# Performance work log

Hardware: AMD Instinct MI355X
Metric: run time of the kernel (lower is better)

The kernel has to match this reference:

```python
import jax, jax.numpy as jnp
import numpy as np
from jax import lax

NMS_SIZE = 5
THR = 0.0
B, C, H, W = 8, 1, 2048, 2048
# fixed capacity for the jit-compatible nonzero (padded with -1); generous upper
# bound on number of surviving local maxima (~HW/25 per map, half above thr=0)
MAX_KEYPOINTS = 2_000_000


def setup_inputs() -> dict:
    key = jax.random.key(0)
    scores = jax.random.normal(key, (B, C, H, W), dtype=jnp.float32)
    return {"scores": scores}


def _local_max(scores):
    # MaxPool2d(kernel=5, stride=1, padding=2) == SAME-padded windowed max
    return lax.reduce_window(
        scores,
        -jnp.inf,
        lax.max,
        window_dimensions=(1, 1, NMS_SIZE, NMS_SIZE),
        window_strides=(1, 1, 1, 1),
        padding="SAME",
    )


def reference(scores):
    maxima = (scores == _local_max(scores)) & (scores > THR)  # [B,C,H,W] bool
    # torch: maxima.nonzero().t()[2:4] -> (row, col) coordinates of survivors.
    # jit-compatible fixed-size nonzero, padded with -1 (extra entries beyond
    # the true count are fill values, matching a compacted index list).
    _, _, hh, ww = jnp.nonzero(maxima, size=MAX_KEYPOINTS, fill_value=-1)
    return jnp.stack([hh, ww])  # [2, MAX_KEYPOINTS] int
```

## Files before the change

kernel.cpp:

```cpp
#include <hip/hip_runtime.h>
#include <stdint.h>
#include <math.h>

#define BATCH 8
#define HH 2048
#define WW 2048
#define NTOT (BATCH * HH * WW)
#define NWORDS (NTOT / 32)
#define R 16
#define NSTRIPS (HH / R)
#define NBLK (NSTRIPS * BATCH)
#define BLK_WORDS (R * WW / 32)
#define MAXK 2000000
#define TAILBLK ((MAXK / 4 + 255) / 256)

__global__ __launch_bounds__(256) void nms_mask(const float* __restrict__ scores,
                                                uint8_t* __restrict__ maskbytes,
                                                int* __restrict__ counts) {
    const int strip = blockIdx.x;
    const int b     = blockIdx.y;
    const int tid   = threadIdx.x;
    const int lane  = tid & 63;
    const int wv    = tid >> 6;
    const int c0    = wv * 512 + lane * 8;
    const int h0    = strip * R;
    const float* img  = scores + (size_t)b * HH * WW;
    const float* colp = img + c0;

    const bool has_l = (c0 != 0);
    const bool has_r = (c0 != WW - 8);

    float win[5][12];

#define LOAD_ROW(PH, hrow)                                                    \
    do {                                                                      \
        const int h_ = (hrow);                                                \
        if ((unsigned)h_ < (unsigned)HH) {                                    \
            const float* p_ = colp + (size_t)h_ * WW;                         \
            float4 a_ = *(const float4*)(p_);                                 \
            float4 b_ = *(const float4*)(p_ + 4);                             \
            win[PH][2] = a_.x; win[PH][3] = a_.y;                             \
            win[PH][4] = a_.z; win[PH][5] = a_.w;                             \
            win[PH][6] = b_.x; win[PH][7] = b_.y;                             \
            win[PH][8] = b_.z; win[PH][9] = b_.w;                             \
            if (has_l) {                                                      \
                float2 hl_ = *(const float2*)(p_ - 2);                        \
                win[PH][0] = hl_.x; win[PH][1] = hl_.y;                       \
            } else { win[PH][0] = -INFINITY; win[PH][1] = -INFINITY; }        \
            if (has_r) {                                                      \
                float2 hr_ = *(const float2*)(p_ + 8);                        \
                win[PH][10] = hr_.x; win[PH][11] = hr_.y;                     \
            } else { win[PH][10] = -INFINITY; win[PH][11] = -INFINITY; }      \
        } else {                                                              \
            _Pragma("unroll")                                                 \
            for (int k_ = 0; k_ < 12; ++k_) win[PH][k_] = -INFINITY;          \
        }                                                                     \
    } while (0)

    LOAD_ROW(0, h0 - 2);
    LOAD_ROW(1, h0 - 1);
    LOAD_ROW(2, h0 + 0);
    LOAD_ROW(3, h0 + 1);

    int pc = 0;
    size_t outbyte = (((size_t)(b * HH + h0) * WW) + c0) >> 3;

#pragma unroll
    for (int i = 0; i < R; ++i) {
        LOAD_ROW((4 + i) % 5, h0 + 2 + i);
        const int CEN = (2 + i) % 5;

        float v[12];
#pragma unroll
        for (int k = 0; k < 12; ++k)
            v[k] = fmaxf(fmaxf(fmaxf(win[0][k], win[1][k]),
                               fmaxf(win[2][k], win[3][k])), win[4][k]);
        float p[11];
#pragma unroll
        for (int k = 0; k < 11; ++k) p[k] = fmaxf(v[k], v[k + 1]);

        uint32_t byte = 0;
#pragma unroll
        for (int j = 0; j < 8; ++j) {
            const float hm = fmaxf(fmaxf(p[j], p[j + 2]), v[j + 4]);
            const float s  = win[CEN][j + 2];
            if ((s == hm) && (s > 0.0f)) byte |= (1u << j);
        }
        maskbytes[outbyte] = (uint8_t)byte;
        outbyte += WW / 8;
        pc += __popc(byte);
    }
#undef LOAD_ROW

#pragma unroll
    for (int d = 32; d >= 1; d >>= 1) pc += __shfl_down(pc, d, 64);
    __shared__ int wsum[4];
    if (lane == 0) wsum[wv] = pc;
    __syncthreads();
    if (tid == 0) counts[b * NSTRIPS + strip] = wsum[0] + wsum[1] + wsum[2] + wsum[3];
}

__device__ __forceinline__ int block_sum(int v, int tid) {
    const int lane = tid & 63, wv = tid >> 6;
#pragma unroll
    for (int d = 32; d >= 1; d >>= 1) v += __shfl_down(v, d, 64);
    __shared__ int ws[4];
    __shared__ int res;
    if (lane == 0) ws[wv] = v;
    __syncthreads();
    if (tid == 0) res = ws[0] + ws[1] + ws[2] + ws[3];
    __syncthreads();
    return res;
}

__global__ __launch_bounds__(256) void compact_tail(const uint32_t* __restrict__ bitmask,
                                                    const int* __restrict__ counts,
                                                    int* __restrict__ out_h,
                                                    int* __restrict__ out_w) {
    const int tid = threadIdx.x;

    if (blockIdx.x >= NBLK) {
        const uint4 c4 = ((const uint4*)counts)[tid];
        int total = block_sum((int)(c4.x + c4.y + c4.z + c4.w), tid);
        if (total < 0) total = 0;
        if (total > MAXK) total = MAXK;

        const int base = ((int)(blockIdx.x - NBLK) * 256 + tid) * 4;
        if (base >= MAXK) return;
        if (base + 4 <= total) return;

        if (base >= total) {
            const int4 neg = make_int4(-1, -1, -1, -1);
            *(int4*)(out_h + base) = neg;
            *(int4*)(out_w + base) = neg;
        } else {
#pragma unroll
            for (int j = 0; j < 4; ++j) {
                const int idx = base + j;
                if (idx >= total) { out_h[idx] = -1; out_w[idx] = -1; }
            }
        }
        return;
    }

    const int chunk = blockIdx.x;

    const uint4 c4 = ((const uint4*)counts)[tid];
    const int i0 = tid * 4;
    int contrib = 0;
    contrib += (i0 + 0 < chunk) ? (int)c4.x : 0;
    contrib += (i0 + 1 < chunk) ? (int)c4.y : 0;
    contrib += (i0 + 2 < chunk) ? (int)c4.z : 0;
    contrib += (i0 + 3 < chunk) ? (int)c4.w : 0;
    const int chunk_base = block_sum(contrib, tid);

    const uint32_t* base = bitmask + (size_t)chunk * BLK_WORDS;
    uint4 m = ((const uint4*)base)[tid];
    uint32_t words[4] = {m.x, m.y, m.z, m.w};
    int pc = __popc(m.x) + __popc(m.y) + __popc(m.z) + __popc(m.w);

    const int lane = tid & 63, wv = tid >> 6;
    int incl = pc;
#pragma unroll
    for (int d = 1; d < 64; d <<= 1) {
        int n = __shfl_up(incl, d, 64);
        if (lane >= d) incl += n;
    }
    __shared__ int wsums[4];
    if (lane == 63) wsums[wv] = incl;
    __syncthreads();
    int wbase = 0;
    for (int i = 0; i < wv; ++i) wbase += wsums[i];

    int off = chunk_base + wbase + (incl - pc);

    uint32_t idx0 = ((uint32_t)chunk * BLK_WORDS + (uint32_t)tid * 4u) * 32u;
#pragma unroll
    for (int wj = 0; wj < 4; ++wj) {
        uint32_t mm = words[wj];
        const uint32_t ib = idx0 + (uint32_t)wj * 32u;
        while (mm) {
            const int bit = __ffs(mm) - 1;
            mm &= mm - 1;
            const uint32_t idx = ib + bit;
            if (off < MAXK) {
                out_h[off] = (int)((idx >> 11) & 2047);
                out_w[off] = (int)(idx & 2047);
            }
            ++off;
        }
    }
}

extern "C" void kernel_launch(void* const* d_in, const int* in_sizes, int n_in,
                              void* d_out, int out_size, void* d_ws, size_t ws_size,
                              hipStream_t stream) {
    const float* scores = (const float*)d_in[0];
    int* out = (int*)d_out;

    uint32_t* bitmask = (uint32_t*)d_ws;
    int* counts = (int*)((char*)d_ws + (size_t)NWORDS * 4);

    nms_mask<<<dim3(NSTRIPS, BATCH), 256, 0, stream>>>(scores, (uint8_t*)bitmask, counts);
    compact_tail<<<NBLK + TAILBLK, 256, 0, stream>>>(bitmask, counts, out, out + MAXK);
}
```

Baseline: 42.90 us.

## Fuse mask and compaction into one kernel with decoupled look-back scan

Merges the NMS mask kernel and the compaction/tail kernel into a single kernel. The bitmask stays in LDS instead of a global workspace, and chunk offsets come from a decoupled look-back prefix scan over atomic flags, with a dynamic chunk id taken from an atomic counter. The -1 tail fill is spread across all blocks after they spin-wait on the last chunk's inclusive total. This removes one launch and the global bitmask round-trip, but adds a memset, spin-waits and serialization along the look-back chain.

```diff
diff --git a/kernel.cpp b/kernel.cpp
--- a/kernel.cpp
+++ b/kernel.cpp
@@ -5,28 +5,41 @@
 #define BATCH 8
 #define HH 2048
 #define WW 2048
-#define NTOT (BATCH * HH * WW)
-#define NWORDS (NTOT / 32)
 #define R 16
 #define NSTRIPS (HH / R)
 #define NBLK (NSTRIPS * BATCH)
-#define BLK_WORDS (R * WW / 32)
+#define CHUNK_DWORDS (R * WW / 32)
 #define MAXK 2000000
-#define TAILBLK ((MAXK / 4 + 255) / 256)
-
-__global__ __launch_bounds__(256) void nms_mask(const float* __restrict__ scores,
-                                                uint8_t* __restrict__ maskbytes,
-                                                int* __restrict__ counts) {
-    const int strip = blockIdx.x;
-    const int b     = blockIdx.y;
-    const int tid   = threadIdx.x;
-    const int lane  = tid & 63;
-    const int wv    = tid >> 6;
+#define TAIL_I4 (MAXK / 4)
+#define TAIL_PER_BLK ((TAIL_I4 + NBLK - 1) / NBLK)
+
+#define STAT_AGG (1u << 30)
+#define STAT_INC (2u << 30)
+#define VALMASK  0x3FFFFFFFu
+
+__global__ __launch_bounds__(256) void nms_fused(const float* __restrict__ scores,
+                                                 uint32_t* __restrict__ flags,
+                                                 int* __restrict__ out_h,
+                                                 int* __restrict__ out_w) {
+    __shared__ uint32_t lds_mask[CHUNK_DWORDS];
+    __shared__ int wsum[4];
+    __shared__ int bcast[2];
+    __shared__ int vbid_s;
+
+    const int tid  = threadIdx.x;
+    const int lane = tid & 63;
+    const int wv   = tid >> 6;
+
+    if (tid == 0) vbid_s = (int)atomicAdd(&flags[NBLK], 1u);
+    __syncthreads();
+    const int chunk = vbid_s;
+
+    const int b     = chunk >> 7;
+    const int strip = chunk & (NSTRIPS - 1);
+    const int h0    = strip * R;
     const int c0    = wv * 512 + lane * 8;
-    const int h0    = strip * R;
     const float* img  = scores + (size_t)b * HH * WW;
     const float* colp = img + c0;
-
     const bool has_l = (c0 != 0);
     const bool has_r = (c0 != WW - 8);
 
@@ -62,8 +75,8 @@
     LOAD_ROW(2, h0 + 0);
     LOAD_ROW(3, h0 + 1);
 
-    int pc = 0;
-    size_t outbyte = (((size_t)(b * HH + h0) * WW) + c0) >> 3;
+    uint8_t* mbytes = (uint8_t*)lds_mask;
+    const int bytecol = wv * 64 + lane;
 
 #pragma unroll
     for (int i = 0; i < R; ++i) {
@@ -86,49 +99,111 @@
             const float s  = win[CEN][j + 2];
             if ((s == hm) && (s > 0.0f)) byte |= (1u << j);
         }
-        maskbytes[outbyte] = (uint8_t)byte;
-        outbyte += WW / 8;
-        pc += __popc(byte);
+        mbytes[i * 256 + bytecol] = (uint8_t)byte;
     }
 #undef LOAD_ROW
 
-#pragma unroll
-    for (int d = 32; d >= 1; d >>= 1) pc += __shfl_down(pc, d, 64);
-    __shared__ int wsum[4];
-    if (lane == 0) wsum[wv] = pc;
-    __syncthreads();
-    if (tid == 0) counts[b * NSTRIPS + strip] = wsum[0] + wsum[1] + wsum[2] + wsum[3];
-}
-
-__device__ __forceinline__ int block_sum(int v, int tid) {
-    const int lane = tid & 63, wv = tid >> 6;
-#pragma unroll
-    for (int d = 32; d >= 1; d >>= 1) v += __shfl_down(v, d, 64);
-    __shared__ int ws[4];
-    __shared__ int res;
-    if (lane == 0) ws[wv] = v;
-    __syncthreads();
-    if (tid == 0) res = ws[0] + ws[1] + ws[2] + ws[3];
-    __syncthreads();
-    return res;
-}
-
-__global__ __launch_bounds__(256) void compact_tail(const uint32_t* __restrict__ bitmask,
-                                                    const int* __restrict__ counts,
-                                                    int* __restrict__ out_h,
-                                                    int* __restrict__ out_w) {
-    const int tid = threadIdx.x;
-
-    if (blockIdx.x >= NBLK) {
-        const uint4 c4 = ((const uint4*)counts)[tid];
-        int total = block_sum((int)(c4.x + c4.y + c4.z + c4.w), tid);
-        if (total < 0) total = 0;
-        if (total > MAXK) total = MAXK;
-
-        const int base = ((int)(blockIdx.x - NBLK) * 256 + tid) * 4;
-        if (base >= MAXK) return;
-        if (base + 4 <= total) return;
-
+    __syncthreads();
+
+    const uint4 m = ((const uint4*)lds_mask)[tid];
+    const int pc = __popc(m.x) + __popc(m.y) + __popc(m.z) + __popc(m.w);
+
+    int red = pc;
+#pragma unroll
+    for (int d = 32; d >= 1; d >>= 1) red += __shfl_down(red, d, 64);
+    if (lane == 0) wsum[wv] = red;
+    __syncthreads();
+    const int agg = wsum[0] + wsum[1] + wsum[2] + wsum[3];
+
+    if (tid == 0) atomicExch(&flags[chunk], STAT_AGG | (uint32_t)agg);
+
+    if (wv == 0) {
+        int exclusive = 0;
+        int look = chunk;
+        while (look > 0) {
+            const int j = look - 1 - lane;
+            const bool valid = (j >= 0);
+            uint32_t f;
+            for (;;) {
+                f = valid ? atomicOr(&flags[j], 0u) : STAT_INC;
+                if (!__any((f >> 30) == 0)) break;
+                __builtin_amdgcn_s_sleep(1);
+            }
+            const unsigned long long m2 = __ballot((f >> 30) == 2);
+            if (m2) {
+                const int stop = (int)__ffsll((unsigned long long)m2) - 1;
+                int c = (lane <= stop) ? (int)(f & VALMASK) : 0;
+#pragma unroll
+                for (int d = 1; d < 64; d <<= 1) c += __shfl_xor(c, d, 64);
+                exclusive += c;
+                break;
+            } else {
+                int c = (int)(f & VALMASK);
+#pragma unroll
+                for (int d = 1; d < 64; d <<= 1) c += __shfl_xor(c, d, 64);
+                exclusive += c;
+                look -= 64;
+            }
+        }
+        if (lane == 0) {
+            bcast[0] = exclusive;
+            atomicExch(&flags[chunk], STAT_INC | (uint32_t)(exclusive + agg));
+        }
+    }
+    __syncthreads();
+    const int chunk_base = bcast[0];
+
+    int incl = pc;
+#pragma unroll
+    for (int d = 1; d < 64; d <<= 1) {
+        int n = __shfl_up(incl, d, 64);
+        if (lane >= d) incl += n;
+    }
+    if (lane == 63) wsum[wv] = incl;
+    __syncthreads();
+    int wbase = 0;
+    for (int i = 0; i < wv; ++i) wbase += wsum[i];
+
+    int off = chunk_base + wbase + (incl - pc);
+
+    uint32_t words[4] = {m.x, m.y, m.z, m.w};
+    const uint32_t local0 = (uint32_t)tid * 128u;
+#pragma unroll
+    for (int wj = 0; wj < 4; ++wj) {
+        uint32_t mm = words[wj];
+        const uint32_t lb = local0 + (uint32_t)wj * 32u;
+        while (mm) {
+            const int bit = __ffs(mm) - 1;
+            mm &= mm - 1;
+            const uint32_t L = lb + (uint32_t)bit;
+            if (off < MAXK) {
+                out_h[off] = h0 + (int)(L >> 11);
+                out_w[off] = (int)(L & 2047u);
+            }
+            ++off;
+        }
+    }
+
+    if (tid == 0) {
+        uint32_t f;
+        for (;;) {
+            f = atomicOr(&flags[NBLK - 1], 0u);
+            if ((f >> 30) == 2) break;
+            __builtin_amdgcn_s_sleep(2);
+        }
+        int t = (int)(f & VALMASK);
+        if (t > MAXK) t = MAXK;
+        bcast[1] = t;
+    }
+    __syncthreads();
+    const int total = bcast[1];
+
+    const int i4base = chunk * TAIL_PER_BLK;
+    for (int t = tid; t < TAIL_PER_BLK; t += 256) {
+        const int i4 = i4base + t;
+        if (i4 >= TAIL_I4) break;
+        const int base = i4 * 4;
+        if (base + 4 <= total) continue;
         if (base >= total) {
             const int4 neg = make_int4(-1, -1, -1, -1);
             *(int4*)(out_h + base) = neg;
@@ -140,55 +215,6 @@
                 if (idx >= total) { out_h[idx] = -1; out_w[idx] = -1; }
             }
         }
-        return;
-    }
-
-    const int chunk = blockIdx.x;
-
-    const uint4 c4 = ((const uint4*)counts)[tid];
-    const int i0 = tid * 4;
-    int contrib = 0;
-    contrib += (i0 + 0 < chunk) ? (int)c4.x : 0;
-    contrib += (i0 + 1 < chunk) ? (int)c4.y : 0;
-    contrib += (i0 + 2 < chunk) ? (int)c4.z : 0;
-    contrib += (i0 + 3 < chunk) ? (int)c4.w : 0;
-    const int chunk_base = block_sum(contrib, tid);
-
-    const uint32_t* base = bitmask + (size_t)chunk * BLK_WORDS;
-    uint4 m = ((const uint4*)base)[tid];
-    uint32_t words[4] = {m.x, m.y, m.z, m.w};
-    int pc = __popc(m.x) + __popc(m.y) + __popc(m.z) + __popc(m.w);
-
-    const int lane = tid & 63, wv = tid >> 6;
-    int incl = pc;
-#pragma unroll
-    for (int d = 1; d < 64; d <<= 1) {
-        int n = __shfl_up(incl, d, 64);
-        if (lane >= d) incl += n;
-    }
-    __shared__ int wsums[4];
-    if (lane == 63) wsums[wv] = incl;
-    __syncthreads();
-    int wbase = 0;
-    for (int i = 0; i < wv; ++i) wbase += wsums[i];
-
-    int off = chunk_base + wbase + (incl - pc);
-
-    uint32_t idx0 = ((uint32_t)chunk * BLK_WORDS + (uint32_t)tid * 4u) * 32u;
-#pragma unroll
-    for (int wj = 0; wj < 4; ++wj) {
-        uint32_t mm = words[wj];
-        const uint32_t ib = idx0 + (uint32_t)wj * 32u;
-        while (mm) {
-            const int bit = __ffs(mm) - 1;
-            mm &= mm - 1;
-            const uint32_t idx = ib + bit;
-            if (off < MAXK) {
-                out_h[off] = (int)((idx >> 11) & 2047);
-                out_w[off] = (int)(idx & 2047);
-            }
-            ++off;
-        }
     }
 }
 
@@ -197,10 +223,9 @@
                               hipStream_t stream) {
     const float* scores = (const float*)d_in[0];
     int* out = (int*)d_out;
-
-    uint32_t* bitmask = (uint32_t*)d_ws;
-    int* counts = (int*)((char*)d_ws + (size_t)NWORDS * 4);
-
-    nms_mask<<<dim3(NSTRIPS, BATCH), 256, 0, stream>>>(scores, (uint8_t*)bitmask, counts);
-    compact_tail<<<NBLK + TAILBLK, 256, 0, stream>>>(bitmask, counts, out, out + MAXK);
+    uint32_t* flags = (uint32_t*)d_ws;
+
+    hipMemsetAsync(flags, 0, (size_t)(NBLK + 1) * sizeof(uint32_t), stream);
+
+    nms_fused<<<NBLK, 256, 0, stream>>>(scores, flags, out, out + MAXK);
 }
```

Result: slower. 75.01 us (+74.9%).

## Move -1 output fill into mask kernel and drop tail blocks from compaction

Applied to the files above, without the earlier changes.

The -1 padding of the whole output buffer now runs as extra blocks of the first (mask) kernel, using int4 stores over a grid-stride loop. The second kernel then only compacts and overwrites the leading entries with coordinates. The aim is to overlap the fill with the memory-bound mask pass and to remove the count reduction and partial-fill logic from the tail blocks. In exchange, the full 16 MB output is always written before being partly rewritten, which adds write traffic compared with filling only past the total count.

```diff
diff --git a/kernel.cpp b/kernel.cpp
--- a/kernel.cpp
+++ b/kernel.cpp
@@ -5,28 +5,37 @@
 #define BATCH 8
 #define HH 2048
 #define WW 2048
-#define NTOT (BATCH * HH * WW)
-#define NWORDS (NTOT / 32)
 #define R 16
 #define NSTRIPS (HH / R)
 #define NBLK (NSTRIPS * BATCH)
 #define BLK_WORDS (R * WW / 32)
 #define MAXK 2000000
-#define TAILBLK ((MAXK / 4 + 255) / 256)
+#define FILLB 1024
+#define OUT_I4 ((2 * MAXK) / 4)
 
-__global__ __launch_bounds__(256) void nms_mask(const float* __restrict__ scores,
-                                                uint8_t* __restrict__ maskbytes,
-                                                int* __restrict__ counts) {
-    const int strip = blockIdx.x;
-    const int b     = blockIdx.y;
-    const int tid   = threadIdx.x;
+__global__ __launch_bounds__(256) void nms_mask_fill(const float* __restrict__ scores,
+                                                     uint8_t* __restrict__ maskbytes,
+                                                     int* __restrict__ counts,
+                                                     int* __restrict__ out) {
+    const int tid  = threadIdx.x;
+
+    if (blockIdx.x >= NBLK) {
+        const int fb = (int)blockIdx.x - NBLK;
+        const int4 neg = make_int4(-1, -1, -1, -1);
+        int4* o = (int4*)out;
+        for (int i = fb * 256 + tid; i < OUT_I4; i += FILLB * 256)
+            o[i] = neg;
+        return;
+    }
+
+    const int chunk = blockIdx.x;
+    const int b     = chunk >> 7;
+    const int strip = chunk & (NSTRIPS - 1);
+    const int h0    = strip * R;
     const int lane  = tid & 63;
     const int wv    = tid >> 6;
     const int c0    = wv * 512 + lane * 8;
-    const int h0    = strip * R;
-    const float* img  = scores + (size_t)b * HH * WW;
-    const float* colp = img + c0;
-
+    const float* colp = scores + (size_t)b * HH * WW + c0;
     const bool has_l = (c0 != 0);
     const bool has_r = (c0 != WW - 8);
 
@@ -97,53 +106,16 @@
     __shared__ int wsum[4];
     if (lane == 0) wsum[wv] = pc;
     __syncthreads();
-    if (tid == 0) counts[b * NSTRIPS + strip] = wsum[0] + wsum[1] + wsum[2] + wsum[3];
+    if (tid == 0) counts[chunk] = wsum[0] + wsum[1] + wsum[2] + wsum[3];
 }
 
-__device__ __forceinline__ int block_sum(int v, int tid) {
-    const int lane = tid & 63, wv = tid >> 6;
-#pragma unroll
-    for (int d = 32; d >= 1; d >>= 1) v += __shfl_down(v, d, 64);
-    __shared__ int ws[4];
-    __shared__ int res;
-    if (lane == 0) ws[wv] = v;
-    __syncthreads();
-    if (tid == 0) res = ws[0] + ws[1] + ws[2] + ws[3];
-    __syncthreads();
-    return res;
-}
-
-__global__ __launch_bounds__(256) void compact_tail(const uint32_t* __restrict__ bitmask,
-                                                    const int* __restrict__ counts,
-                                                    int* __restrict__ out_h,
-                                                    int* __restrict__ out_w) {
-    const int tid = threadIdx.x;
-
-    if (blockIdx.x >= NBLK) {
-        const uint4 c4 = ((const uint4*)counts)[tid];
-        int total = block_sum((int)(c4.x + c4.y + c4.z + c4.w), tid);
-        if (total < 0) total = 0;
-        if (total > MAXK) total = MAXK;
-
-        const int base = ((int)(blockIdx.x - NBLK) * 256 + tid) * 4;
-        if (base >= MAXK) return;
-        if (base + 4 <= total) return;
-
-        if (base >= total) {
-            const int4 neg = make_int4(-1, -1, -1, -1);
-            *(int4*)(out_h + base) = neg;
-            *(int4*)(out_w + base) = neg;
-        } else {
-#pragma unroll
-            for (int j = 0; j < 4; ++j) {
-                const int idx = base + j;
-                if (idx >= total) { out_h[idx] = -1; out_w[idx] = -1; }
-            }
-        }
-        return;
-    }
-
+__global__ __launch_bounds__(256) void compact(const uint32_t* __restrict__ bitmask,
+                                               const int* __restrict__ counts,
+                                               int* __restrict__ out_h,
+                                               int* __restrict__ out_w) {
     const int chunk = blockIdx.x;
+    const int tid   = threadIdx.x;
+    const int lane  = tid & 63, wv = tid >> 6;
 
     const uint4 c4 = ((const uint4*)counts)[tid];
     const int i0 = tid * 4;
@@ -152,14 +124,20 @@
     contrib += (i0 + 1 < chunk) ? (int)c4.y : 0;
     contrib += (i0 + 2 < chunk) ? (int)c4.z : 0;
     contrib += (i0 + 3 < chunk) ? (int)c4.w : 0;
-    const int chunk_base = block_sum(contrib, tid);
 
-    const uint32_t* base = bitmask + (size_t)chunk * BLK_WORDS;
-    uint4 m = ((const uint4*)base)[tid];
-    uint32_t words[4] = {m.x, m.y, m.z, m.w};
-    int pc = __popc(m.x) + __popc(m.y) + __popc(m.z) + __popc(m.w);
+    int red = contrib;
+#pragma unroll
+    for (int d = 32; d >= 1; d >>= 1) red += __shfl_down(red, d, 64);
+    __shared__ int ws[4];
+    __shared__ int base_s;
+    if (lane == 0) ws[wv] = red;
+    __syncthreads();
+    if (tid == 0) base_s = ws[0] + ws[1] + ws[2] + ws[3];
 
-    const int lane = tid & 63, wv = tid >> 6;
+    const uint32_t* mbase = bitmask + (size_t)chunk * BLK_WORDS;
+    const uint4 m = ((const uint4*)mbase)[tid];
+    const int pc = __popc(m.x) + __popc(m.y) + __popc(m.z) + __popc(m.w);
+
     int incl = pc;
 #pragma unroll
     for (int d = 1; d < 64; d <<= 1) {
@@ -172,20 +150,22 @@
     int wbase = 0;
     for (int i = 0; i < wv; ++i) wbase += wsums[i];
 
-    int off = chunk_base + wbase + (incl - pc);
+    const int h0 = (chunk & (NSTRIPS - 1)) * R;
+    int off = base_s + wbase + (incl - pc);
 
-    uint32_t idx0 = ((uint32_t)chunk * BLK_WORDS + (uint32_t)tid * 4u) * 32u;
+    uint32_t words[4] = {m.x, m.y, m.z, m.w};
+    const uint32_t local0 = (uint32_t)tid * 128u;
 #pragma unroll
     for (int wj = 0; wj < 4; ++wj) {
         uint32_t mm = words[wj];
-        const uint32_t ib = idx0 + (uint32_t)wj * 32u;
+        const uint32_t lb = local0 + (uint32_t)wj * 32u;
         while (mm) {
             const int bit = __ffs(mm) - 1;
             mm &= mm - 1;
-            const uint32_t idx = ib + bit;
+            const uint32_t L = lb + (uint32_t)bit;
             if (off < MAXK) {
-                out_h[off] = (int)((idx >> 11) & 2047);
-                out_w[off] = (int)(idx & 2047);
+                out_h[off] = h0 + (int)(L >> 11);
+                out_w[off] = (int)(L & 2047u);
             }
             ++off;
         }
@@ -199,8 +179,9 @@
     int* out = (int*)d_out;
 
     uint32_t* bitmask = (uint32_t*)d_ws;
-    int* counts = (int*)((char*)d_ws + (size_t)NWORDS * 4);
+    int* counts = (int*)((char*)d_ws + (size_t)NBLK * BLK_WORDS * 4);
 
-    nms_mask<<<dim3(NSTRIPS, BATCH), 256, 0, stream>>>(scores, (uint8_t*)bitmask, counts);
-    compact_tail<<<NBLK + TAILBLK, 256, 0, stream>>>(bitmask, counts, out, out + MAXK);
+    nms_mask_fill<<<NBLK + FILLB, 256, 0, stream>>>(scores, (uint8_t*)bitmask,
+                                                    counts, out);
+    compact<<<NBLK, 256, 0, stream>>>(bitmask, counts, out, out + MAXK);
 }
```

Measured after the change: 43.14 us. Within noise of the previous version (+0.6%).
